# Kernel tuning notes

Hardware: AMD Instinct MI355X
Metric: run time of the kernel (lower is better)

The kernel has to match this reference:

```python
import jax, jax.numpy as jnp
import numpy as np


def _expm_batch(S):
    # S: [..., m, m] skew-symmetric -> elementwise matrix exponential
    flat = S.reshape((-1,) + S.shape[-2:])
    E = jax.vmap(jax.scipy.linalg.expm)(flat)
    return E.reshape(S.shape)


def _time_prod(M):
    # M: [B, T, m, m] -> Z = M[:,T-1] @ ... @ M[:,0]  (dyadic, log-depth, matches DevNet dyadic_prod order)
    B, T, m, _ = M.shape
    eye = jnp.eye(m, dtype=M.dtype)
    while M.shape[1] > 1:
        if M.shape[1] % 2 == 1:
            pad = jnp.broadcast_to(eye, (B, 1, m, m))
            M = jnp.concatenate([M, pad], axis=1)
        # later factor on the left: M[:,1::2] @ M[:,0::2]
        M = jnp.einsum('btij,btjk->btik', M[:, 1::2], M[:, 0::2])
    return M[:, 0]


def setup_inputs() -> dict:
    key = jax.random.key(0)
    k1, k2, k3 = jax.random.split(key, 3)
    B, T, Cin, m, O = 64, 2048, 8, 16, 10
    X = jax.random.normal(k1, (B, T, Cin), dtype=jnp.float32)
    A = jax.random.normal(k2, (m, m, Cin), dtype=jnp.float32) * 0.2
    W = jax.random.normal(k3, (O, m * m), dtype=jnp.float32) * (1.0 / np.sqrt(m * m))
    b = jnp.zeros((O,), dtype=jnp.float32)
    return {"X": X, "A": A, "W": W, "b": b}


def reference(X, A, W, b):
    # skew-symmetric parametrization of the Lie algebra so(m)
    A_skew = A - jnp.swapaxes(A, 0, 1)          # [m, m, Cin]
    dX = X[:, 1:] - X[:, :-1]                    # [B, T-1, Cin] path increments
    S = jnp.einsum('btc,ijc->btij', dX, A_skew)  # [B, T-1, m, m] skew per step
    M = _expm_batch(S)                           # per-step SO(m) elements
    Z = _time_prod(M)                            # [B, m, m] path development
    out = Z.reshape(Z.shape[0], -1) @ W.T + b    # [B, n_outputs]
    return out
```

## Files before the change

### kernel.cpp

```cpp
#include <hip/hip_runtime.h>

#define BSZ   64
#define TLEN  2048
#define NSTEP 2047
#define CIN   8
#define NCH   128
#define CHL   16

typedef __attribute__((ext_vector_type(4))) float    fx4;
typedef __attribute__((ext_vector_type(4))) _Float16 hx4;

__device__ __forceinline__ hx4 pk4(float a, float b, float c, float d) {
    auto p0 = __builtin_amdgcn_cvt_pkrtz(a, b);
    auto p1 = __builtin_amdgcn_cvt_pkrtz(c, d);
    hx4 r; r[0] = p0[0]; r[1] = p0[1]; r[2] = p1[0]; r[3] = p1[1];
    return r;
}

__device__ __forceinline__ void splitf(const fx4 v, hx4& hi, hx4& lo) {
    _Float16 h0 = (_Float16)v[0], h1 = (_Float16)v[1];
    _Float16 h2 = (_Float16)v[2], h3 = (_Float16)v[3];
    hi[0] = h0; hi[1] = h1; hi[2] = h2; hi[3] = h3;
    lo = pk4(v[0] - (float)h0, v[1] - (float)h1, v[2] - (float)h2, v[3] - (float)h3);
}

__device__ __forceinline__ fx4 mm3(hx4 ah, hx4 al, hx4 bh, hx4 bl) {
    fx4 acc = {0.f, 0.f, 0.f, 0.f};
    acc = __builtin_amdgcn_mfma_f32_16x16x16f16(ah, bh, acc, 0, 0, 0);
    acc = __builtin_amdgcn_mfma_f32_16x16x16f16(ah, bl, acc, 0, 0, 0);
    acc = __builtin_amdgcn_mfma_f32_16x16x16f16(al, bh, acc, 0, 0, 0);
    return acc;
}

__device__ __forceinline__ void mfmaT(hx4 Mh, hx4 Ml, hx4 Ih, hx4& Th, hx4& Tl) {
    fx4 z = {0.f, 0.f, 0.f, 0.f};
    fx4 th = __builtin_amdgcn_mfma_f32_16x16x16f16(Mh, Ih, z, 0, 0, 0);
    fx4 tl = __builtin_amdgcn_mfma_f32_16x16x16f16(Ml, Ih, z, 0, 0, 0);
    Th = pk4(th[0], th[1], th[2], th[3]);
    Tl = pk4(tl[0], tl[1], tl[2], tl[3]);
}

__device__ __forceinline__ fx4 foldQ(fx4 Q, fx4 Acc, hx4 Ih) {
    hx4 Qh, Ql, Th, Tl, Bh, Bl;
    splitf(Q, Qh, Ql);
    mfmaT(Qh, Ql, Ih, Th, Tl);
    splitf(Acc, Bh, Bl);
    return mm3(Th, Tl, Bh, Bl);
}

__device__ __forceinline__ float infnorm(fx4 sv) {
    float a = fabsf(sv[0]) + fabsf(sv[1]) + fabsf(sv[2]) + fabsf(sv[3]);
    a += __shfl_xor(a, 16, 64);
    a += __shfl_xor(a, 32, 64);
    a = fmaxf(a, __shfl_xor(a, 1, 64));
    a = fmaxf(a, __shfl_xor(a, 2, 64));
    a = fmaxf(a, __shfl_xor(a, 4, 64));
    a = fmaxf(a, __shfl_xor(a, 8, 64));
    return a;
}

__device__ __forceinline__ void loadDx(const float* __restrict__ X, int b, int t,
                                       float dx[CIN]) {
    if (t < NSTEP) {
        const float* xp = X + ((size_t)b * TLEN + t) * CIN;
        const float4 x0 = *reinterpret_cast<const float4*>(xp + 0);
        const float4 x1 = *reinterpret_cast<const float4*>(xp + 4);
        const float4 y0 = *reinterpret_cast<const float4*>(xp + 8);
        const float4 y1 = *reinterpret_cast<const float4*>(xp + 12);
        dx[0] = y0.x - x0.x; dx[1] = y0.y - x0.y; dx[2] = y0.z - x0.z; dx[3] = y0.w - x0.w;
        dx[4] = y1.x - x1.x; dx[5] = y1.y - x1.y; dx[6] = y1.z - x1.z; dx[7] = y1.w - x1.w;
    } else {
#pragma unroll
        for (int i = 0; i < CIN; ++i) dx[i] = 0.f;
    }
}

__global__ __launch_bounds__(256, 4)
void devnet_expm_chunk(const float* __restrict__ X, const float* __restrict__ A,
                       float* __restrict__ G)
{
    const int tid  = threadIdx.x;
    const int wid  = tid >> 6;
    const int lane = tid & 63;
    const int m    = lane >> 4;
    const int c    = lane & 15;
    const int gw   = blockIdx.x * 4 + wid;
    const int b    = gw >> 6;
    const int ch0  = gw & 63;

    float ask[4][CIN];
#pragma unroll
    for (int r = 0; r < 4; ++r) {
        const int i = 4 * m + r;
#pragma unroll
        for (int cc = 0; cc < CIN; ++cc)
            ask[r][cc] = A[(i * 16 + c) * CIN + cc] - A[(c * 16 + i) * CIN + cc];
    }

    fx4 idv;
#pragma unroll
    for (int r = 0; r < 4; ++r) idv[r] = (4 * m + r == c) ? 1.f : 0.f;
    const hx4 Ih = pk4(idv[0], idv[1], idv[2], idv[3]);

    fx4 P0 = idv, P1 = idv;

    for (int tt = 0; tt < CHL; ++tt) {
        const int ta = ch0 * CHL + tt;
        const int tb = (ch0 + 64) * CHL + tt;

        float dxa[CIN], dxb[CIN];
        loadDx(X, b, ta, dxa);
        loadDx(X, b, tb, dxb);

        fx4 sa, sb;
#pragma unroll
        for (int r = 0; r < 4; ++r) {
            float va = 0.f, vb = 0.f;
#pragma unroll
            for (int cc = 0; cc < CIN; ++cc) {
                va = fmaf(dxa[cc], ask[r][cc], va);
                vb = fmaf(dxb[cc], ask[r][cc], vb);
            }
            sa[r] = va; sb[r] = vb;
        }

        const float na = infnorm(sa);
        const float nb = infnorm(sb);
        int ea, eb;
        (void)frexpf(na, &ea);
        (void)frexpf(nb, &eb);
        int sc = (ea > eb ? ea : eb) + 2;
        if (sc < 0) sc = 0;
        const float scale = ldexpf(1.0f, -sc);

        fx4 xa = sa * scale, xb = sb * scale;
        hx4 XahA, XalA, XahB, XalB;
        {
            fx4 nxa = -xa, nxb = -xb;
            splitf(nxa, XahA, XalA);
            splitf(nxb, XahB, XalB);
        }

        fx4 Ra, Rb;
#pragma unroll
        for (int r = 0; r < 4; ++r) {
            Ra[r] = fmaf(xa[r], 0.2f, idv[r]);
            Rb[r] = fmaf(xb[r], 0.2f, idv[r]);
        }
#pragma unroll
        for (int k = 4; k >= 1; --k) {
            hx4 RhA, RlA, RhB, RlB;
            splitf(Ra, RhA, RlA);
            splitf(Rb, RhB, RlB);
            fx4 qa = mm3(XahA, XalA, RhA, RlA);
            fx4 qb = mm3(XahB, XalB, RhB, RlB);
            const float inv = 1.f / (float)k;
#pragma unroll
            for (int r = 0; r < 4; ++r) {
                Ra[r] = fmaf(qa[r], inv, idv[r]);
                Rb[r] = fmaf(qb[r], inv, idv[r]);
            }
        }

        for (int q = 0; q < sc; ++q) {
            hx4 RhA, RlA, ThA, TlA, RhB, RlB, ThB, TlB;
            splitf(Ra, RhA, RlA);
            splitf(Rb, RhB, RlB);
            mfmaT(RhA, RlA, Ih, ThA, TlA);
            mfmaT(RhB, RlB, Ih, ThB, TlB);
            Ra = mm3(ThA, TlA, RhA, RlA);
            Rb = mm3(ThB, TlB, RhB, RlB);
        }

        P0 = foldQ(Ra, P0, Ih);
        P1 = foldQ(Rb, P1, Ih);
    }

    float* gp = G + ((size_t)b * NCH) * 256;
    *reinterpret_cast<fx4*>(gp + (size_t)ch0 * 256 + lane * 4)        = P0;
    *reinterpret_cast<fx4*>(gp + (size_t)(ch0 + 64) * 256 + lane * 4) = P1;
}

__global__ __launch_bounds__(256)
void devnet_reduce(const float* __restrict__ G, const float* __restrict__ W,
                   const float* __restrict__ bias, float* __restrict__ out)
{
    __shared__ __align__(16) float Fs[4][256];
    __shared__ float Zf[256];

    const int tid  = threadIdx.x;
    const int wid  = tid >> 6;
    const int lane = tid & 63;
    const int m    = lane >> 4;
    const int c    = lane & 15;
    const int b    = blockIdx.x;

    fx4 idv;
#pragma unroll
    for (int r = 0; r < 4; ++r) idv[r] = (4 * m + r == c) ? 1.f : 0.f;
    const hx4 Ih = pk4(idv[0], idv[1], idv[2], idv[3]);

    const float* gb    = G + (size_t)b * NCH * 256;
    const float* baseA = gb + (size_t)(wid * 32) * 256;
    const float* baseB = gb + (size_t)(wid * 32 + 16) * 256;

    fx4 AccA = *reinterpret_cast<const fx4*>(baseA + lane * 4);
    fx4 AccB = *reinterpret_cast<const fx4*>(baseB + lane * 4);
    for (int k = 1; k < 16; ++k) {
        fx4 Qa = *reinterpret_cast<const fx4*>(baseA + (size_t)k * 256 + lane * 4);
        fx4 Qb = *reinterpret_cast<const fx4*>(baseB + (size_t)k * 256 + lane * 4);
        AccA = foldQ(Qa, AccA, Ih);
        AccB = foldQ(Qb, AccB, Ih);
    }
    fx4 Acc = foldQ(AccB, AccA, Ih);
    *reinterpret_cast<fx4*>(&Fs[wid][lane * 4]) = Acc;
    __syncthreads();

    if (wid == 0) {
        fx4 Z = *reinterpret_cast<const fx4*>(&Fs[0][lane * 4]);
        for (int w = 1; w < 4; ++w) {
            fx4 Q = *reinterpret_cast<const fx4*>(&Fs[w][lane * 4]);
            Z = foldQ(Q, Z, Ih);
        }
#pragma unroll
        for (int r = 0; r < 4; ++r) Zf[(4 * m + r) * 16 + c] = Z[r];

        for (int o = 0; o < 10; ++o) {
            const float* wo = W + o * 256;
            float v = Zf[lane] * wo[lane];
            v = fmaf(Zf[lane + 64],  wo[lane + 64],  v);
            v = fmaf(Zf[lane + 128], wo[lane + 128], v);
            v = fmaf(Zf[lane + 192], wo[lane + 192], v);
#pragma unroll
            for (int off = 32; off >= 1; off >>= 1) v += __shfl_down(v, off, 64);
            if (lane == 0) out[b * 10 + o] = v + bias[o];
        }
    }
}

extern "C" void kernel_launch(void* const* d_in, const int* in_sizes, int n_in,
                              void* d_out, int out_size, void* d_ws, size_t ws_size,
                              hipStream_t stream)
{
    const float* X    = (const float*)d_in[0];
    const float* A    = (const float*)d_in[1];
    const float* W    = (const float*)d_in[2];
    const float* bias = (const float*)d_in[3];
    float* out = (float*)d_out;
    float* G   = (float*)d_ws;

    devnet_expm_chunk<<<BSZ * NCH / 8, 256, 0, stream>>>(X, A, G);
    devnet_reduce<<<BSZ, 256, 0, stream>>>(G, W, bias, out);
}
```

Baseline: 180.8 us.

## Use per-matrix squaring counts, MFMA row-sum norm, and wider reduce kernel

```diff
diff --git a/kernel.cpp b/kernel.cpp
--- a/kernel.cpp
+++ b/kernel.cpp
@@ -48,14 +48,13 @@
     return mm3(Th, Tl, Bh, Bl);
 }
 
-__device__ __forceinline__ float infnorm(fx4 sv) {
-    float a = fabsf(sv[0]) + fabsf(sv[1]) + fabsf(sv[2]) + fabsf(sv[3]);
-    a += __shfl_xor(a, 16, 64);
-    a += __shfl_xor(a, 32, 64);
-    a = fmaxf(a, __shfl_xor(a, 1, 64));
-    a = fmaxf(a, __shfl_xor(a, 2, 64));
-    a = fmaxf(a, __shfl_xor(a, 4, 64));
-    a = fmaxf(a, __shfl_xor(a, 8, 64));
+__device__ __forceinline__ float infnormS(fx4 s, hx4 Oh) {
+    hx4 sab = pk4(fabsf(s[0]), fabsf(s[1]), fabsf(s[2]), fabsf(s[3]));
+    fx4 z = {0.f, 0.f, 0.f, 0.f};
+    fx4 rs = __builtin_amdgcn_mfma_f32_16x16x16f16(sab, Oh, z, 0, 0, 0);
+    float a = fmaxf(fmaxf(rs[0], rs[1]), fmaxf(rs[2], rs[3]));
+    a = fmaxf(a, __shfl_xor(a, 16, 64));
+    a = fmaxf(a, __shfl_xor(a, 32, 64));
     return a;
 }
 
@@ -101,6 +100,7 @@
 #pragma unroll
     for (int r = 0; r < 4; ++r) idv[r] = (4 * m + r == c) ? 1.f : 0.f;
     const hx4 Ih = pk4(idv[0], idv[1], idv[2], idv[3]);
+    const hx4 Oh = pk4(1.f, 1.f, 1.f, 1.f);
 
     fx4 P0 = idv, P1 = idv;
 
@@ -124,16 +124,18 @@
             sa[r] = va; sb[r] = vb;
         }
 
-        const float na = infnorm(sa);
-        const float nb = infnorm(sb);
+        const float na = infnormS(sa, Oh);
+        const float nb = infnormS(sb, Oh);
+
         int ea, eb;
         (void)frexpf(na, &ea);
         (void)frexpf(nb, &eb);
-        int sc = (ea > eb ? ea : eb) + 2;
-        if (sc < 0) sc = 0;
-        const float scale = ldexpf(1.0f, -sc);
-
-        fx4 xa = sa * scale, xb = sb * scale;
+        int sca = ea + 2; if (sca < 0) sca = 0;
+        int scb = eb + 2; if (scb < 0) scb = 0;
+        const float sclA = ldexpf(1.0f, -sca);
+        const float sclB = ldexpf(1.0f, -scb);
+
+        fx4 xa = sa * sclA, xb = sb * sclB;
         hx4 XahA, XalA, XahB, XalB;
         {
             fx4 nxa = -xa, nxb = -xb;
@@ -162,14 +164,20 @@
             }
         }
 
-        for (int q = 0; q < sc; ++q) {
-            hx4 RhA, RlA, ThA, TlA, RhB, RlB, ThB, TlB;
-            splitf(Ra, RhA, RlA);
-            splitf(Rb, RhB, RlB);
-            mfmaT(RhA, RlA, Ih, ThA, TlA);
-            mfmaT(RhB, RlB, Ih, ThB, TlB);
-            Ra = mm3(ThA, TlA, RhA, RlA);
-            Rb = mm3(ThB, TlB, RhB, RlB);
+        const int scm = (sca > scb) ? sca : scb;
+        for (int q = 0; q < scm; ++q) {
+            if (q < sca) {
+                hx4 Rh, Rl, Th, Tl;
+                splitf(Ra, Rh, Rl);
+                mfmaT(Rh, Rl, Ih, Th, Tl);
+                Ra = mm3(Th, Tl, Rh, Rl);
+            }
+            if (q < scb) {
+                hx4 Rh, Rl, Th, Tl;
+                splitf(Rb, Rh, Rl);
+                mfmaT(Rh, Rl, Ih, Th, Tl);
+                Rb = mm3(Th, Tl, Rh, Rl);
+            }
         }
 
         P0 = foldQ(Ra, P0, Ih);
@@ -181,11 +189,11 @@
     *reinterpret_cast<fx4*>(gp + (size_t)(ch0 + 64) * 256 + lane * 4) = P1;
 }
 
-__global__ __launch_bounds__(256)
+__global__ __launch_bounds__(512)
 void devnet_reduce(const float* __restrict__ G, const float* __restrict__ W,
                    const float* __restrict__ bias, float* __restrict__ out)
 {
-    __shared__ __align__(16) float Fs[4][256];
+    __shared__ __align__(16) float Fs[8][256];
     __shared__ float Zf[256];
 
     const int tid  = threadIdx.x;
@@ -201,12 +209,13 @@
     const hx4 Ih = pk4(idv[0], idv[1], idv[2], idv[3]);
 
     const float* gb    = G + (size_t)b * NCH * 256;
-    const float* baseA = gb + (size_t)(wid * 32) * 256;
-    const float* baseB = gb + (size_t)(wid * 32 + 16) * 256;
+    const float* baseA = gb + (size_t)(wid * 16) * 256;
+    const float* baseB = gb + (size_t)(wid * 16 + 8) * 256;
 
     fx4 AccA = *reinterpret_cast<const fx4*>(baseA + lane * 4);
     fx4 AccB = *reinterpret_cast<const fx4*>(baseB + lane * 4);
-    for (int k = 1; k < 16; ++k) {
+#pragma unroll
+    for (int k = 1; k < 8; ++k) {
         fx4 Qa = *reinterpret_cast<const fx4*>(baseA + (size_t)k * 256 + lane * 4);
         fx4 Qb = *reinterpret_cast<const fx4*>(baseB + (size_t)k * 256 + lane * 4);
         AccA = foldQ(Qa, AccA, Ih);
@@ -218,7 +227,8 @@
 
     if (wid == 0) {
         fx4 Z = *reinterpret_cast<const fx4*>(&Fs[0][lane * 4]);
-        for (int w = 1; w < 4; ++w) {
+#pragma unroll
+        for (int w = 1; w < 8; ++w) {
             fx4 Q = *reinterpret_cast<const fx4*>(&Fs[w][lane * 4]);
             Z = foldQ(Q, Z, Ih);
         }
@@ -250,5 +260,5 @@
     float* G   = (float*)d_ws;
 
     devnet_expm_chunk<<<BSZ * NCH / 8, 256, 0, stream>>>(X, A, G);
-    devnet_reduce<<<BSZ, 256, 0, stream>>>(G, W, bias, out);
-}
+    devnet_reduce<<<BSZ, 512, 0, stream>>>(G, W, bias, out);
+}
```

Result: no change. 177.9 us (-1.6%).
